# Kernel tuning notes

Measured on AMD Instinct MI355X. Metric: run time of the kernel, lower is better.

## Reference

```python
import jax, jax.numpy as jnp
import numpy as np

D_IN = 2048
D_OUT = 2048
NUM_HEADS = 16
HEAD_DIM = D_OUT // NUM_HEADS


def setup_inputs() -> dict:
    key = jax.random.key(0)
    k_x, k_qkv, k_proj, k_b = jax.random.split(key, 4)
    x = jax.random.normal(k_x, (2, 2048, D_IN), dtype=jnp.float32)
    # torch Linear(d_in, 3*d_out, bias=False): weight [3*d_out, d_in]; store transposed [d_in, 3*d_out]
    Wqkv = jax.random.normal(k_qkv, (D_IN, 3 * D_OUT), dtype=jnp.float32) / np.sqrt(D_IN)
    Wproj = jax.random.normal(k_proj, (D_OUT, D_OUT), dtype=jnp.float32) / np.sqrt(D_OUT)
    bproj = jax.random.normal(k_b, (D_OUT,), dtype=jnp.float32) * 0.01
    return {"x": x, "Wqkv": Wqkv, "Wproj": Wproj, "bproj": bproj}


def reference(x, Wqkv, Wproj, bproj):
    B, S, _ = x.shape
    qkv = x @ Wqkv  # [B, S, 3*D_OUT]
    qkv = qkv.reshape(B, S, 3, NUM_HEADS, HEAD_DIM)
    qkv = jnp.transpose(qkv, (2, 0, 3, 1, 4))  # [3, B, H, S, Dh]
    q, k, v = qkv[0], qkv[1], qkv[2]
    scale = 1.0 / np.sqrt(HEAD_DIM).astype(np.float32)
    scores = jnp.einsum('bhqd,bhkd->bhqk', q, k) * scale  # [B, H, S, S]
    causal = jnp.tril(jnp.ones((S, S), dtype=bool))
    scores = jnp.where(causal, scores, jnp.finfo(scores.dtype).min)
    attn = jax.nn.softmax(scores, axis=-1)
    out = jnp.einsum('bhqk,bhkd->bhqd', attn, v)  # [B, H, S, Dh]
    out = jnp.transpose(out, (0, 2, 1, 3)).reshape(B, S, D_OUT)
    return out @ Wproj + bproj
```

## Files before the change

kernel.cpp:

```cpp
#include <hip/hip_runtime.h>
#include <stdint.h>

typedef __attribute__((ext_vector_type(8))) short short8;
typedef __attribute__((ext_vector_type(4))) float f32x4;
typedef __attribute__((ext_vector_type(16))) float f32x16;
typedef __attribute__((ext_vector_type(4))) unsigned short u16x4;

typedef unsigned short u16;

constexpr int S_LEN = 2048;
constexpr int DH    = 128;

__device__ __forceinline__ u16 f2bf(float f) {
    union { float f; unsigned u; } v; v.f = f;
    unsigned r = v.u + 0x7FFFu + ((v.u >> 16) & 1u);
    return (u16)(r >> 16);
}
__device__ __forceinline__ void gl_lds16(const void* g, void* l) {
    __builtin_amdgcn_global_load_lds((const __attribute__((address_space(1))) void*)g,
                                     (__attribute__((address_space(3))) void*)l,
                                     16, 0, 0);
}

__global__ __launch_bounds__(256) void convx(const float* __restrict__ src,
                                             u16* __restrict__ dst) {
    size_t i = ((size_t)blockIdx.x * 256 + threadIdx.x) * 8;
    f32x4 a = *(const f32x4*)(src + i);
    f32x4 b = *(const f32x4*)(src + i + 4);
    short8 r;
    r[0] = (short)f2bf(a[0]); r[1] = (short)f2bf(a[1]);
    r[2] = (short)f2bf(a[2]); r[3] = (short)f2bf(a[3]);
    r[4] = (short)f2bf(b[0]); r[5] = (short)f2bf(b[1]);
    r[6] = (short)f2bf(b[2]); r[7] = (short)f2bf(b[3]);
    *(short8*)(dst + i) = r;
}

__global__ void convT(const float* __restrict__ src, u16* __restrict__ dst,
                      int rows, int cols) {
    __shared__ u16 tile[32][33];
    int c0 = blockIdx.x * 32, r0 = blockIdx.y * 32;
    int tx = threadIdx.x, ty = threadIdx.y;
#pragma unroll
    for (int i = 0; i < 32; i += 8)
        tile[ty + i][tx] = f2bf(src[(size_t)(r0 + ty + i) * cols + c0 + tx]);
    __syncthreads();
#pragma unroll
    for (int i = 0; i < 32; i += 8)
        dst[(size_t)(c0 + ty + i) * rows + r0 + tx] = tile[tx][ty + i];
}

__global__ __launch_bounds__(256) void gemm_qkv(
        const u16* __restrict__ A, const u16* __restrict__ BT,
        u16* __restrict__ Qo, u16* __restrict__ Ko, u16* __restrict__ VTo) {
    __shared__ __align__(16) u16 lA[128 * 32];
    __shared__ __align__(16) u16 lB[128 * 32];
    const int tid = threadIdx.x;
    const int lane = tid & 63, wave = tid >> 6;
    const int quad = lane >> 4, l16 = lane & 15;
    const int wm = wave >> 1, wn = wave & 1;
    const int m0 = blockIdx.y * 128, n0 = blockIdx.x * 128;
    f32x4 acc[4][4] = {};
    const int rbase = tid >> 2;
    const int cofs  = (tid & 3) * 8;

    for (int k0 = 0; k0 < 2048; k0 += 32) {
#pragma unroll
        for (int it = 0; it < 2; ++it) {
            int row = it * 64 + rbase;
            gl_lds16(A  + (size_t)(m0 + row) * 2048 + k0 + cofs, &lA[(it * 256 + tid) * 8]);
            gl_lds16(BT + (size_t)(n0 + row) * 2048 + k0 + cofs, &lB[(it * 256 + tid) * 8]);
        }
        __syncthreads();
        short8 af[4], bf[4];
#pragma unroll
        for (int i = 0; i < 4; ++i) {
            af[i] = *(const short8*)&lA[(wm * 64 + i * 16 + l16) * 32 + quad * 8];
            bf[i] = *(const short8*)&lB[(wn * 64 + i * 16 + l16) * 32 + quad * 8];
        }
#pragma unroll
        for (int im = 0; im < 4; ++im)
#pragma unroll
            for (int in = 0; in < 4; ++in)
                acc[im][in] = __builtin_amdgcn_mfma_f32_16x16x32_bf16(af[im], bf[in], acc[im][in], 0, 0, 0);
        __syncthreads();
    }
#pragma unroll
    for (int im = 0; im < 4; ++im) {
        int r0r = m0 + wm * 64 + im * 16 + quad * 4;
        int b = r0r >> 11, s0 = r0r & 2047;
#pragma unroll
        for (int in = 0; in < 4; ++in) {
            int cc = n0 + wn * 64 + in * 16 + l16;
            int which = cc >> 11, hd = (cc >> 7) & 15, dh = cc & 127;
            if (which < 2) {
                u16* dst = which == 0 ? Qo : Ko;
#pragma unroll
                for (int rg = 0; rg < 4; ++rg)
                    dst[(size_t)((b * 16 + hd) * 2048 + s0 + rg) * 128 + dh] = f2bf(acc[im][in][rg]);
            } else {
                u16x4 v;
#pragma unroll
                for (int rg = 0; rg < 4; ++rg) v[rg] = f2bf(acc[im][in][rg]);
                *(u16x4*)&VTo[((size_t)(b * 16 + hd) * 128 + dh) * 2048 + s0] = v;
            }
        }
    }
}

__global__ __launch_bounds__(256, 2) void attn_kern(
        u16* __restrict__ QOp, const u16* __restrict__ Kp,
        const u16* __restrict__ VTp) {
    __shared__ __align__(16) u16 lK[2][64 * 128];
    __shared__ __align__(16) u16 lV[2][128 * 64];
    const int tid = threadIdx.x, lane = tid & 63, wave = tid >> 6;
    const int ql = lane & 31, hi = lane >> 5;
    const int qb = 15 - blockIdx.x, bh = blockIdx.y;
    const int qbase = qb * 128 + wave * 32;
    const int qmax = qbase + 31;
    const int nkt = 2 * qb + 2;
    u16* Qh = QOp + (size_t)bh * S_LEN * DH;
    const u16* Kh = Kp + (size_t)bh * S_LEN * DH;
    const u16* VTh = VTp + (size_t)bh * DH * S_LEN;

    short8 qf[8];
#pragma unroll
    for (int c = 0; c < 8; ++c)
        qf[c] = *(const short8*)&Qh[(size_t)(qbase + ql) * 128 + c * 16 + hi * 8];

    f32x16 acc[4] = {};
    float mrun = -1e30f, lrun = 0.f;
    const float SC = 0.08838834764831845f * 1.44269504088896f;

    auto stage = [&](int kt, int b) {
        const u16* ks = Kh + (size_t)kt * 64 * 128;
#pragma unroll
        for (int p = 0; p < 4; ++p) {
            int slot = p * 256 + tid;
            int row = slot >> 4, c4 = slot & 15;
            gl_lds16(ks + row * 128 + ((c4 ^ (row & 15)) * 8), &lK[b][slot * 8]);
        }
        const u16* vs = VTh + kt * 64;
#pragma unroll
        for (int p = 0; p < 4; ++p) {
            int slot = p * 256 + tid;
            int row = slot >> 3, c4 = slot & 7;
            gl_lds16(vs + (size_t)row * 2048 + ((c4 ^ (row & 7)) * 8), &lV[b][slot * 8]);
        }
    };

    stage(0, 0);
    __syncthreads();

    for (int kt = 0; kt < nkt; ++kt) {
        const int buf = kt & 1;
        if (kt + 1 < nkt) stage(kt + 1, buf ^ 1);
        if (kt * 64 <= qmax) {
            const bool part = (kt * 64 + 63 > qbase);
            f32x16 s0 = {}, s1 = {};
#pragma unroll
            for (int c = 0; c < 8; ++c) {
                int sl = ((c * 2 + hi) ^ (ql & 15)) * 8;
                short8 k0 = *(const short8*)&lK[buf][ql * 128 + sl];
                short8 k1 = *(const short8*)&lK[buf][(32 + ql) * 128 + sl];
                s0 = __builtin_amdgcn_mfma_f32_32x32x16_bf16(k0, qf[c], s0, 0, 0, 0);
                s1 = __builtin_amdgcn_mfma_f32_32x32x16_bf16(k1, qf[c], s1, 0, 0, 0);
            }
            float pv0[16], pv1[16];
            float pm = -1e30f;
            const int qg = qbase + ql;
#pragma unroll
            for (int r = 0; r < 16; ++r) {
                int krow = (r & 3) + 8 * (r >> 2) + 4 * hi;
                float a = s0[r] * SC;
                float b = s1[r] * SC;
                if (part) {
                    if (kt * 64 + krow > qg)      a = -1e30f;
                    if (kt * 64 + 32 + krow > qg) b = -1e30f;
                }
                pv0[r] = a; pv1[r] = b;
                pm = fmaxf(pm, fmaxf(a, b));
            }
            pm = fmaxf(pm, __shfl_xor(pm, 32));
            if (__any(pm - mrun > 8.f)) {
                float mn = fmaxf(mrun, pm);
                float al = exp2f(mrun - mn);
                mrun = mn;
                lrun *= al;
#pragma unroll
                for (int r = 0; r < 16; ++r) {
                    float ar = __shfl(al, (r & 3) + 8 * (r >> 2) + 4 * hi);
#pragma unroll
                    for (int dc = 0; dc < 4; ++dc)
                        acc[dc][r] *= ar;
                }
            }
            float rs = 0.f;
#pragma unroll
            for (int r = 0; r < 16; ++r) {
                pv0[r] = exp2f(pv0[r] - mrun);
                pv1[r] = exp2f(pv1[r] - mrun);
                rs += pv0[r] + pv1[r];
            }
            rs += __shfl_xor(rs, 32);
            lrun += rs;
            unsigned X0[8], X1[8];
#pragma unroll
            for (int i = 0; i < 8; ++i) {
                X0[i] = (unsigned)f2bf(pv0[2 * i]) | ((unsigned)f2bf(pv0[2 * i + 1]) << 16);
                X1[i] = (unsigned)f2bf(pv1[2 * i]) | ((unsigned)f2bf(pv1[2 * i + 1]) << 16);
            }
            short8 pa[4];
#pragma unroll
            for (int t = 0; t < 2; ++t)
#pragma unroll
                for (int h = 0; h < 2; ++h) {
                    unsigned x0 = t ? X1[4 * h + 0] : X0[4 * h + 0];
                    unsigned x1 = t ? X1[4 * h + 1] : X0[4 * h + 1];
                    unsigned x2 = t ? X1[4 * h + 2] : X0[4 * h + 2];
                    unsigned x3 = t ? X1[4 * h + 3] : X0[4 * h + 3];
                    unsigned sx0 = (unsigned)__shfl_xor((int)x0, 32);
                    unsigned sx1 = (unsigned)__shfl_xor((int)x1, 32);
                    unsigned sx2 = (unsigned)__shfl_xor((int)x2, 32);
                    unsigned sx3 = (unsigned)__shfl_xor((int)x3, 32);
                    union { unsigned u[4]; short8 s; } uf;
                    uf.u[0] = hi ? sx2 : x0;
                    uf.u[1] = hi ? sx3 : x1;
                    uf.u[2] = hi ? x2 : sx0;
                    uf.u[3] = hi ? x3 : sx1;
                    pa[t * 2 + h] = uf.s;
                }
#pragma unroll
            for (int dc = 0; dc < 4; ++dc) {
                const int rv = dc * 32 + ql;
#pragma unroll
                for (int kc = 0; kc < 4; ++kc) {
                    short8 vf = *(const short8*)&lV[buf][rv * 64 + (((kc * 2 + hi) ^ (ql & 7)) * 8)];
                    acc[dc] = __builtin_amdgcn_mfma_f32_32x32x16_bf16(pa[kc], vf, acc[dc], 0, 0, 0);
                }
            }
        }
        __syncthreads();
    }

    float linv = 1.f / lrun;
#pragma unroll
    for (int r = 0; r < 16; ++r) {
        int qr = (r & 3) + 8 * (r >> 2) + 4 * hi;
        float lr = __shfl(linv, qr);
        int qq = qbase + qr;
#pragma unroll
        for (int dc = 0; dc < 4; ++dc)
            Qh[(size_t)qq * 128 + dc * 32 + ql] = f2bf(acc[dc][r] * lr);
    }
}

__global__ __launch_bounds__(256) void gemm_proj(
        const u16* __restrict__ QO, const u16* __restrict__ BT,
        const float* __restrict__ bias, float* __restrict__ out) {
    __shared__ __align__(16) u16 lA[128 * 32];
    __shared__ __align__(16) u16 lB[128 * 32];
    const int tid = threadIdx.x;
    const int lane = tid & 63, wave = tid >> 6;
    const int quad = lane >> 4, l16 = lane & 15;
    const int wm = wave >> 1, wn = wave & 1;
    const int m0 = blockIdx.y * 128, n0 = blockIdx.x * 128;
    f32x4 acc[4][4] = {};
    const int rbase = tid >> 2;
    const int cofs  = (tid & 3) * 8;

    for (int k0 = 0; k0 < 2048; k0 += 32) {
#pragma unroll
        for (int it = 0; it < 2; ++it) {
            int row = m0 + it * 64 + rbase;
            int b = row >> 11, s = row & 2047;
            int k = k0 + cofs, h = k >> 7, dh = k & 127;
            gl_lds16(QO + ((size_t)(b * 16 + h) * 2048 + s) * 128 + dh, &lA[(it * 256 + tid) * 8]);
            gl_lds16(BT + (size_t)(n0 + it * 64 + rbase) * 2048 + k0 + cofs, &lB[(it * 256 + tid) * 8]);
        }
        __syncthreads();
        short8 af[4], bf[4];
#pragma unroll
        for (int i = 0; i < 4; ++i) {
            af[i] = *(const short8*)&lA[(wm * 64 + i * 16 + l16) * 32 + quad * 8];
            bf[i] = *(const short8*)&lB[(wn * 64 + i * 16 + l16) * 32 + quad * 8];
        }
#pragma unroll
        for (int im = 0; im < 4; ++im)
#pragma unroll
            for (int in = 0; in < 4; ++in)
                acc[im][in] = __builtin_amdgcn_mfma_f32_16x16x32_bf16(af[im], bf[in], acc[im][in], 0, 0, 0);
        __syncthreads();
    }
#pragma unroll
    for (int im = 0; im < 4; ++im) {
        int r0r = m0 + wm * 64 + im * 16 + quad * 4;
#pragma unroll
        for (int in = 0; in < 4; ++in) {
            int cc = n0 + wn * 64 + in * 16 + l16;
            float bv = bias[cc];
#pragma unroll
            for (int rg = 0; rg < 4; ++rg)
                out[(size_t)(r0r + rg) * 2048 + cc] = acc[im][in][rg] + bv;
        }
    }
}

extern "C" void kernel_launch(void* const* d_in, const int* in_sizes, int n_in,
                              void* d_out, int out_size, void* d_ws, size_t ws_size,
                              hipStream_t stream) {
    const float *x = nullptr, *Wqkv = nullptr, *Wproj = nullptr, *bproj = nullptr;
    for (int i = 0; i < n_in; ++i) {
        int sz = in_sizes[i];
        if      (sz == 2 * 2048 * 2048) x     = (const float*)d_in[i];
        else if (sz == 2048 * 6144)     Wqkv  = (const float*)d_in[i];
        else if (sz == 2048 * 2048)     Wproj = (const float*)d_in[i];
        else if (sz == 2048)            bproj = (const float*)d_in[i];
    }
    float* out = (float*)d_out;

    u16* xb     = (u16*)d_ws;
    u16* WqkvT  = xb    + (size_t)4096 * 2048;
    u16* Qb     = WqkvT + (size_t)6144 * 2048;
    u16* Kb     = Qb    + (size_t)32 * 2048 * 128;
    u16* VTb    = Kb    + (size_t)32 * 2048 * 128;
    u16* WprojT = xb;

    convx<<<dim3(4096), dim3(256), 0, stream>>>(x, xb);
    convT<<<dim3(192, 64), dim3(32, 8), 0, stream>>>(Wqkv, WqkvT, 2048, 6144);
    gemm_qkv<<<dim3(48, 32), dim3(256), 0, stream>>>(xb, WqkvT, Qb, Kb, VTb);
    convT<<<dim3(64, 64), dim3(32, 8), 0, stream>>>(Wproj, WprojT, 2048, 2048);
    attn_kern<<<dim3(16, 32), dim3(256), 0, stream>>>(Qb, Kb, VTb);
    gemm_proj<<<dim3(16, 32), dim3(256), 0, stream>>>(Qb, WprojT, bproj, out);
}
```

Baseline: 419.5 us.

## Rewrite QKV GEMM with 256x256 tiles, double-buffered swizzled LDS and phased prefetch

```diff
diff --git a/kernel.cpp b/kernel.cpp
--- a/kernel.cpp
+++ b/kernel.cpp
@@ -49,58 +49,102 @@
         dst[(size_t)(c0 + ty + i) * rows + r0 + tx] = tile[tx][ty + i];
 }
 
-__global__ __launch_bounds__(256) void gemm_qkv(
+__global__ __launch_bounds__(512, 2) void gemm_qkv(
         const u16* __restrict__ A, const u16* __restrict__ BT,
         u16* __restrict__ Qo, u16* __restrict__ Ko, u16* __restrict__ VTo) {
-    __shared__ __align__(16) u16 lA[128 * 32];
-    __shared__ __align__(16) u16 lB[128 * 32];
+    __shared__ __align__(16) u16 lA[2][256 * 64];
+    __shared__ __align__(16) u16 lB[2][256 * 64];
     const int tid = threadIdx.x;
     const int lane = tid & 63, wave = tid >> 6;
     const int quad = lane >> 4, l16 = lane & 15;
-    const int wm = wave >> 1, wn = wave & 1;
-    const int m0 = blockIdx.y * 128, n0 = blockIdx.x * 128;
-    f32x4 acc[4][4] = {};
-    const int rbase = tid >> 2;
-    const int cofs  = (tid & 3) * 8;
-
-    for (int k0 = 0; k0 < 2048; k0 += 32) {
-#pragma unroll
-        for (int it = 0; it < 2; ++it) {
-            int row = it * 64 + rbase;
-            gl_lds16(A  + (size_t)(m0 + row) * 2048 + k0 + cofs, &lA[(it * 256 + tid) * 8]);
-            gl_lds16(BT + (size_t)(n0 + row) * 2048 + k0 + cofs, &lB[(it * 256 + tid) * 8]);
-        }
-        __syncthreads();
-        short8 af[4], bf[4];
-#pragma unroll
-        for (int i = 0; i < 4; ++i) {
-            af[i] = *(const short8*)&lA[(wm * 64 + i * 16 + l16) * 32 + quad * 8];
-            bf[i] = *(const short8*)&lB[(wn * 64 + i * 16 + l16) * 32 + quad * 8];
-        }
-#pragma unroll
-        for (int im = 0; im < 4; ++im)
-#pragma unroll
-            for (int in = 0; in < 4; ++in)
-                acc[im][in] = __builtin_amdgcn_mfma_f32_16x16x32_bf16(af[im], bf[in], acc[im][in], 0, 0, 0);
-        __syncthreads();
-    }
-#pragma unroll
-    for (int im = 0; im < 4; ++im) {
-        int r0r = m0 + wm * 64 + im * 16 + quad * 4;
+    const int wr = wave >> 2, wc = wave & 3;
+    const int m0 = blockIdx.y * 256, n0 = blockIdx.x * 256;
+    const int sw = l16 & 7;
+    const int c4 = tid & 7;
+    const int rih0 = tid >> 3;
+    f32x4 acc[8][4] = {};
+
+    auto stageA = [&](int h, int t1, int nb) {
+#pragma unroll
+        for (int j = 0; j < 2; ++j) {
+            int rih = j * 64 + rih0;
+            int row = (rih & 63) + h * 64 + (rih >> 6) * 128;
+            gl_lds16(A + (size_t)(m0 + row) * 2048 + t1 * 64 + ((c4 ^ (row & 7)) * 8),
+                     &lA[nb][row * 64 + c4 * 8]);
+        }
+    };
+    auto stageB = [&](int h, int t1, int nb) {
+#pragma unroll
+        for (int j = 0; j < 2; ++j) {
+            int rih = j * 64 + rih0;
+            int row = (rih & 31) + h * 32 + (rih >> 5) * 64;
+            gl_lds16(BT + (size_t)(n0 + row) * 2048 + t1 * 64 + ((c4 ^ (row & 7)) * 8),
+                     &lB[nb][row * 64 + c4 * 8]);
+        }
+    };
+
+    stageA(0, 0, 0); stageB(0, 0, 0); stageA(1, 0, 0); stageB(1, 0, 0);
+    asm volatile("s_waitcnt vmcnt(4)\n\ts_barrier" ::: "memory");
+
+    constexpr int NT = 32;
+    for (int t = 0; t < NT; ++t) {
+        const int buf = t & 1, nb = buf ^ 1;
+        const bool pf = (t + 1 < NT);
+#pragma unroll
+        for (int ph = 0; ph < 4; ++ph) {
+            const int qm = ph & 1, qn = ph >> 1;
+            short8 af[4][2], bfr[2][2];
+            const int abase = (wr * 128 + qm * 64 + l16) * 64;
+            const int bbase = (wc * 64 + qn * 32 + l16) * 64;
+#pragma unroll
+            for (int m = 0; m < 4; ++m)
+#pragma unroll
+                for (int ks = 0; ks < 2; ++ks)
+                    af[m][ks] = *(const short8*)&lA[buf][abase + m * 1024 + (((ks * 4 + quad) ^ sw)) * 8];
+#pragma unroll
+            for (int n = 0; n < 2; ++n)
+#pragma unroll
+                for (int ks = 0; ks < 2; ++ks)
+                    bfr[n][ks] = *(const short8*)&lB[buf][bbase + n * 1024 + (((ks * 4 + quad) ^ sw)) * 8];
+            if (pf) {
+                if      (ph == 0) stageA(0, t + 1, nb);
+                else if (ph == 1) stageB(0, t + 1, nb);
+                else if (ph == 2) stageA(1, t + 1, nb);
+                else              stageB(1, t + 1, nb);
+            }
+            __builtin_amdgcn_s_setprio(1);
+#pragma unroll
+            for (int m = 0; m < 4; ++m)
+#pragma unroll
+                for (int n = 0; n < 2; ++n)
+#pragma unroll
+                    for (int ks = 0; ks < 2; ++ks)
+                        acc[qm * 4 + m][qn * 2 + n] = __builtin_amdgcn_mfma_f32_16x16x32_bf16(
+                            af[m][ks], bfr[n][ks], acc[qm * 4 + m][qn * 2 + n], 0, 0, 0);
+            __builtin_amdgcn_s_setprio(0);
+            if (pf)             asm volatile("s_waitcnt vmcnt(4)\n\ts_barrier" ::: "memory");
+            else if (ph == 0)   asm volatile("s_waitcnt vmcnt(2)\n\ts_barrier" ::: "memory");
+            else                asm volatile("s_waitcnt vmcnt(0)\n\ts_barrier" ::: "memory");
+        }
+    }
+
+#pragma unroll
+    for (int m8 = 0; m8 < 8; ++m8) {
+        int r0r = m0 + wr * 128 + m8 * 16 + quad * 4;
         int b = r0r >> 11, s0 = r0r & 2047;
 #pragma unroll
-        for (int in = 0; in < 4; ++in) {
-            int cc = n0 + wn * 64 + in * 16 + l16;
+        for (int n4 = 0; n4 < 4; ++n4) {
+            int cc = n0 + wc * 64 + n4 * 16 + l16;
             int which = cc >> 11, hd = (cc >> 7) & 15, dh = cc & 127;
             if (which < 2) {
                 u16* dst = which == 0 ? Qo : Ko;
 #pragma unroll
                 for (int rg = 0; rg < 4; ++rg)
-                    dst[(size_t)((b * 16 + hd) * 2048 + s0 + rg) * 128 + dh] = f2bf(acc[im][in][rg]);
+                    dst[(size_t)((b * 16 + hd) * 2048 + s0 + rg) * 128 + dh] = f2bf(acc[m8][n4][rg]);
             } else {
                 u16x4 v;
 #pragma unroll
-                for (int rg = 0; rg < 4; ++rg) v[rg] = f2bf(acc[im][in][rg]);
+                for (int rg = 0; rg < 4; ++rg) v[rg] = f2bf(acc[m8][n4][rg]);
                 *(u16x4*)&VTo[((size_t)(b * 16 + hd) * 128 + dh) * 2048 + s0] = v;
             }
         }
@@ -114,7 +158,8 @@
     __shared__ __align__(16) u16 lV[2][128 * 64];
     const int tid = threadIdx.x, lane = tid & 63, wave = tid >> 6;
     const int ql = lane & 31, hi = lane >> 5;
-    const int qb = 15 - blockIdx.x, bh = blockIdx.y;
+    const int qb = (blockIdx.y < 8) ? (15 - (int)blockIdx.y) : ((int)blockIdx.y - 8);
+    const int bh = blockIdx.x;
     const int qbase = qb * 128 + wave * 32;
     const int qmax = qbase + 31;
     const int nkt = 2 * qb + 2;
@@ -157,6 +202,7 @@
         if (kt * 64 <= qmax) {
             const bool part = (kt * 64 + 63 > qbase);
             f32x16 s0 = {}, s1 = {};
+            __builtin_amdgcn_s_setprio(1);
 #pragma unroll
             for (int c = 0; c < 8; ++c) {
                 int sl = ((c * 2 + hi) ^ (ql & 15)) * 8;
@@ -165,6 +211,7 @@
                 s0 = __builtin_amdgcn_mfma_f32_32x32x16_bf16(k0, qf[c], s0, 0, 0, 0);
                 s1 = __builtin_amdgcn_mfma_f32_32x32x16_bf16(k1, qf[c], s1, 0, 0, 0);
             }
+            __builtin_amdgcn_s_setprio(0);
             float pv0[16], pv1[16];
             float pm = -1e30f;
             const int qg = qbase + ql;
@@ -229,6 +276,7 @@
                     uf.u[3] = hi ? x3 : sx1;
                     pa[t * 2 + h] = uf.s;
                 }
+            __builtin_amdgcn_s_setprio(1);
 #pragma unroll
             for (int dc = 0; dc < 4; ++dc) {
                 const int rv = dc * 32 + ql;
@@ -238,6 +286,7 @@
                     acc[dc] = __builtin_amdgcn_mfma_f32_32x32x16_bf16(pa[kc], vf, acc[dc], 0, 0, 0);
                 }
             }
+            __builtin_amdgcn_s_setprio(0);
         }
         __syncthreads();
     }
@@ -327,8 +376,8 @@
 
     convx<<<dim3(4096), dim3(256), 0, stream>>>(x, xb);
     convT<<<dim3(192, 64), dim3(32, 8), 0, stream>>>(Wqkv, WqkvT, 2048, 6144);
-    gemm_qkv<<<dim3(48, 32), dim3(256), 0, stream>>>(xb, WqkvT, Qb, Kb, VTb);
+    gemm_qkv<<<dim3(24, 16), dim3(512), 0, stream>>>(xb, WqkvT, Qb, Kb, VTb);
     convT<<<dim3(64, 64), dim3(32, 8), 0, stream>>>(Wproj, WprojT, 2048, 2048);
-    attn_kern<<<dim3(16, 32), dim3(256), 0, stream>>>(Qb, Kb, VTb);
+    attn_kern<<<dim3(32, 16), dim3(256), 0, stream>>>(Qb, Kb, VTb);
     gemm_proj<<<dim3(16, 32), dim3(256), 0, stream>>>(Qb, WprojT, bproj, out);
 }
```

After: 428.4 us. 2.1% more time.
